# Kernel tuning notes

Measured on AMD Instinct MI355X. Metric: run time of the kernel, lower is better.

## Reference

```python
import jax, jax.numpy as jnp
import numpy as np

N_POINTS = 2097152
N_LEVELS = 16
F_PER_LEVEL = 2
LOG2_T = 19
T = 1 << LOG2_T            # 524288 entries per level
BASE_RES = 16
GROWTH = 1.5
PRIME_Y = np.uint32(2654435761)  # tcnn 2D spatial-hash prime (dim 0 prime is 1)


def _level_encode(x, tab, level):
    """Bilinear hash-grid lookup for one level. x: [N,2] in [0,1], tab: [T,F]."""
    scale = BASE_RES * GROWTH ** level - 1.0          # python float, static
    res = int(np.ceil(scale)) + 1                     # grid resolution (static)
    dense = res * res <= T                            # tcnn: dense if grid fits

    pos = x * jnp.asarray(scale, x.dtype) + 0.5       # [N,2]
    pg = jnp.floor(pos)
    frac = pos - pg                                   # [N,2] interpolation weights
    pg = pg.astype(jnp.uint32)

    out = jnp.zeros((x.shape[0], F_PER_LEVEL), x.dtype)
    for dx in (0, 1):
        for dy in (0, 1):
            cx = pg[:, 0] + np.uint32(dx)
            cy = pg[:, 1] + np.uint32(dy)
            if dense:
                idx = (cx + cy * np.uint32(res)) % np.uint32(T)
            else:
                idx = (cx ^ (cy * PRIME_Y)) % np.uint32(T)
            wx = frac[:, 0] if dx else 1.0 - frac[:, 0]
            wy = frac[:, 1] if dy else 1.0 - frac[:, 1]
            out = out + tab[idx.astype(jnp.int32)] * (wx * wy)[:, None]
    return out  # [N, F]


def setup_inputs() -> dict:
    key = jax.random.key(0)
    k1, k2 = jax.random.split(key)
    x = jax.random.uniform(k1, (N_POINTS, 2), dtype=jnp.float32)
    # tcnn initializes hash-grid params uniform in [-1e-4, 1e-4]
    table = jax.random.uniform(k2, (N_LEVELS, T, F_PER_LEVEL), dtype=jnp.float32,
                               minval=-1e-4, maxval=1e-4)
    return {"x": x, "table": table}


def reference(x, table):
    # multiresolution hash encoding: per-level bilinear gather, concat features
    outs = [_level_encode(x, table[l], l) for l in range(N_LEVELS)]
    return jnp.concatenate(outs, axis=-1)  # [N, N_LEVELS * F_PER_LEVEL] = [N, 32]
```

## Files before the change

### kernel.cpp

```cpp
#include <hip/hip_runtime.h>
#include <stdint.h>


constexpr int      kNPoints = 2097152;
constexpr uint32_t kT       = 524288u;
constexpr uint32_t kTMask   = kT - 1u;
constexpr uint32_t kPrimeY  = 2654435761u;

typedef float vf4 __attribute__((ext_vector_type(4)));

__device__ __forceinline__ float2 nt_load_f2(const float2* p) {
    union { unsigned long long u; float2 f2; } u;
    u.u = __builtin_nontemporal_load(reinterpret_cast<const unsigned long long*>(p));
    return u.f2;
}

__device__ __forceinline__ void nt_store_f2(float2* p, float2 v) {
    union { unsigned long long u; float2 f2; } u; u.f2 = v;
    __builtin_nontemporal_store(u.u, reinterpret_cast<unsigned long long*>(p));
}

__device__ __forceinline__ void nt_store_f4(float* p, float a, float b, float c, float d) {
    vf4 v; v.x = a; v.y = b; v.z = c; v.w = d;
    __builtin_nontemporal_store(v, reinterpret_cast<vf4*>(p));
}

__device__ __host__ inline void level_consts(int l, float& sc, uint32_t& re, int& dense) {
    const float ksc[16] = {
        15.0f, 23.0f, 35.0f, 53.0f, 80.0f, 120.5f, 181.25f, 272.375f,
        409.0625f, 614.09375f, 921.640625f, 1382.9609375f,
        2074.94140625f, 3112.912109375f, 4669.8681640625f, 7005.30224609375f};
    const uint32_t kre[16] = {16u, 24u, 36u, 54u, 81u, 122u, 183u, 274u,
                              411u, 616u, 923u, 1384u, 2076u, 3114u, 4671u, 7007u};
    sc = ksc[l]; re = kre[l]; dense = (l < 10) ? 1 : 0;
}

__device__ __forceinline__ float2 encode_one(float2 xy, float scale, uint32_t res,
                                             int dense, const float2* __restrict__ tab) {
    const float px  = __fadd_rn(__fmul_rn(xy.x, scale), 0.5f);
    const float py  = __fadd_rn(__fmul_rn(xy.y, scale), 0.5f);
    const float fpx = floorf(px);
    const float fpy = floorf(py);
    const float fx  = px - fpx;
    const float fy  = py - fpy;
    const uint32_t gx = (uint32_t)fpx;
    const uint32_t gy = (uint32_t)fpy;

    float ax = 0.0f, ay = 0.0f;
#pragma unroll
    for (int dx = 0; dx < 2; ++dx) {
        const uint32_t cx = gx + (uint32_t)dx;
        const float    wx = dx ? fx : (1.0f - fx);
#pragma unroll
        for (int dy = 0; dy < 2; ++dy) {
            const uint32_t cy = gy + (uint32_t)dy;
            const float    wy = dy ? fy : (1.0f - fy);
            const uint32_t idx_d = (cx + cy * res) & kTMask;
            const uint32_t idx_h = (cx ^ (cy * kPrimeY)) & kTMask;
            const uint32_t idx   = dense ? idx_d : idx_h;
            const float2   v     = tab[idx];
            const float    w     = wx * wy;
            ax = fmaf(v.x, w, ax);
            ay = fmaf(v.y, w, ay);
        }
    }
    return make_float2(ax, ay);
}

__global__ __launch_bounds__(256) void hash8_kernel(
    const float* __restrict__ x,
    const float* __restrict__ table,
    float2* __restrict__ ws)
{
    const uint32_t slot  = blockIdx.x & 7u;
    const uint32_t chunk = blockIdx.x >> 3;
    const int      l     = 8 + (int)slot;
    float sc; uint32_t re; int de;
    level_consts(l, sc, re, de);
    const float2* __restrict__ tab =
        reinterpret_cast<const float2*>(table) + ((size_t)l << 19);
    float2* __restrict__ wsl = ws + (size_t)slot * kNPoints;

    const uint32_t base = chunk * 1024u + threadIdx.x;
    const float2* __restrict__ xv = reinterpret_cast<const float2*>(x);

    float2 xy[4];
#pragma unroll
    for (int k = 0; k < 4; ++k)
        xy[k] = nt_load_f2(xv + base + (uint32_t)k * 256u);

    float2 r[4];
#pragma unroll
    for (int k = 0; k < 4; ++k)
        r[k] = encode_one(xy[k], sc, re, de, tab);

#pragma unroll
    for (int k = 0; k < 4; ++k)
        nt_store_f2(wsl + base + (uint32_t)k * 256u, r[k]);
}

__global__ __launch_bounds__(256) void merge8_kernel(
    const float* __restrict__ x,
    const float* __restrict__ table,
    const float2* __restrict__ ws,
    float* __restrict__ out)
{
    __shared__ float s[128 * 36];
    const uint32_t tid = threadIdx.x;
    const uint32_t n   = blockIdx.x * 256u + tid;
    const float2   xy  = nt_load_f2(reinterpret_cast<const float2*>(x) + n);

    float2 r[16];
#pragma unroll
    for (int l = 0; l < 8; ++l) {
        float sc; uint32_t re; int de;
        level_consts(l, sc, re, de);
        const float2* tab = reinterpret_cast<const float2*>(table) + ((size_t)l << 19);
        r[l] = encode_one(xy, sc, re, de, tab);
    }
#pragma unroll
    for (int j = 0; j < 8; ++j)
        r[8 + j] = nt_load_f2(ws + (size_t)j * kNPoints + n);

#pragma unroll
    for (int h = 0; h < 2; ++h) {
        if ((tid >> 7) == (uint32_t)h) {
            const uint32_t p = tid & 127u;
#pragma unroll
            for (int l = 0; l < 16; ++l) {
                s[p * 36 + 2 * l]     = r[l].x;
                s[p * 36 + 2 * l + 1] = r[l].y;
            }
        }
        __syncthreads();
        float* ob = out + (size_t)blockIdx.x * 8192 + (uint32_t)h * 4096u;
#pragma unroll
        for (int k = 0; k < 4; ++k) {
            const uint32_t q   = tid + (uint32_t)k * 256u;
            const uint32_t row = q >> 3;
            const uint32_t c   = (q & 7u) * 4u;
            const float* sp = &s[row * 36 + c];
            nt_store_f4(ob + q * 4u, sp[0], sp[1], sp[2], sp[3]);
        }
        if (h == 0) __syncthreads();
    }
}

__global__ __launch_bounds__(256) void hashgrid_fwd_fallback(
    const float* __restrict__ x,
    const float* __restrict__ table,
    float* __restrict__ out)
{
    const uint32_t tid = blockIdx.x * blockDim.x + threadIdx.x;
    const uint32_t l   = tid & 15u;
    const uint32_t n   = tid >> 4;
    float sc; uint32_t re; int de;
    level_consts((int)l, sc, re, de);
    const float2 xy = reinterpret_cast<const float2*>(x)[n];
    const float2* tab = reinterpret_cast<const float2*>(table) + ((size_t)l << 19);
    const float2 r = encode_one(xy, sc, re, de, tab);
    reinterpret_cast<float2*>(out)[tid] = r;
}

extern "C" void kernel_launch(void* const* d_in, const int* in_sizes, int n_in,
                              void* d_out, int out_size, void* d_ws, size_t ws_size,
                              hipStream_t stream) {
    const float* x     = (const float*)d_in[0];
    const float* table = (const float*)d_in[1];
    float*       out   = (float*)d_out;

    const size_t need8 = (size_t)8 * kNPoints * sizeof(float2);

    if (ws_size >= need8) {
        float2* ws = (float2*)d_ws;
        hash8_kernel<<<16384, 256, 0, stream>>>(x, table, ws);
        merge8_kernel<<<kNPoints / 256, 256, 0, stream>>>(x, table, ws, out);
    } else {
        hashgrid_fwd_fallback<<<(kNPoints * 16) / 256, 256, 0, stream>>>(x, table, out);
    }
}
```

Baseline: 686.8 us.

## Use paired 16-byte loads for dense levels and single-pass LDS transpose

For dense levels, the x and x+1 corners are now fetched together as one 16-byte load per row, cutting four gathers to two. Hashed levels compute the corner indices with a shared prime product and issue all gathers before any accumulation. The merge kernel now stages all 256 points in a larger LDS tile with a single barrier. It also drops the nontemporal hints on x, workspace and output accesses. The paired load assumes the two adjacent entries never wrap past the table mask, which holds for these dense resolutions. The larger LDS tile may lower occupancy.

Result: slower. 732.4 us (+6.6%).

```diff
diff --git a/kernel.cpp b/kernel.cpp
--- a/kernel.cpp
+++ b/kernel.cpp
@@ -7,8 +7,6 @@
 constexpr uint32_t kTMask   = kT - 1u;
 constexpr uint32_t kPrimeY  = 2654435761u;
 
-typedef float vf4 __attribute__((ext_vector_type(4)));
-
 __device__ __forceinline__ float2 nt_load_f2(const float2* p) {
     union { unsigned long long u; float2 f2; } u;
     u.u = __builtin_nontemporal_load(reinterpret_cast<const unsigned long long*>(p));
@@ -20,9 +18,11 @@
     __builtin_nontemporal_store(u.u, reinterpret_cast<unsigned long long*>(p));
 }
 
-__device__ __forceinline__ void nt_store_f4(float* p, float a, float b, float c, float d) {
-    vf4 v; v.x = a; v.y = b; v.z = c; v.w = d;
-    __builtin_nontemporal_store(v, reinterpret_cast<vf4*>(p));
+struct PairLd { float2 lo, hi; };
+__device__ __forceinline__ PairLd load_pair(const float2* __restrict__ p) {
+    PairLd r;
+    __builtin_memcpy(&r, p, 16);
+    return r;
 }
 
 __device__ __host__ inline void level_consts(int l, float& sc, uint32_t& re, int& dense) {
@@ -35,35 +35,43 @@
     sc = ksc[l]; re = kre[l]; dense = (l < 10) ? 1 : 0;
 }
 
-__device__ __forceinline__ float2 encode_one(float2 xy, float scale, uint32_t res,
-                                             int dense, const float2* __restrict__ tab) {
+__device__ __forceinline__ void setup_pt(float2 xy, float scale,
+                                         uint32_t& gx, uint32_t& gy,
+                                         float& fx, float& fy) {
     const float px  = __fadd_rn(__fmul_rn(xy.x, scale), 0.5f);
     const float py  = __fadd_rn(__fmul_rn(xy.y, scale), 0.5f);
     const float fpx = floorf(px);
     const float fpy = floorf(py);
-    const float fx  = px - fpx;
-    const float fy  = py - fpy;
-    const uint32_t gx = (uint32_t)fpx;
-    const uint32_t gy = (uint32_t)fpy;
-
-    float ax = 0.0f, ay = 0.0f;
-#pragma unroll
-    for (int dx = 0; dx < 2; ++dx) {
-        const uint32_t cx = gx + (uint32_t)dx;
-        const float    wx = dx ? fx : (1.0f - fx);
-#pragma unroll
-        for (int dy = 0; dy < 2; ++dy) {
-            const uint32_t cy = gy + (uint32_t)dy;
-            const float    wy = dy ? fy : (1.0f - fy);
-            const uint32_t idx_d = (cx + cy * res) & kTMask;
-            const uint32_t idx_h = (cx ^ (cy * kPrimeY)) & kTMask;
-            const uint32_t idx   = dense ? idx_d : idx_h;
-            const float2   v     = tab[idx];
-            const float    w     = wx * wy;
-            ax = fmaf(v.x, w, ax);
-            ay = fmaf(v.y, w, ay);
-        }
-    }
+    fx = px - fpx;
+    fy = py - fpy;
+    gx = (uint32_t)fpx;
+    gy = (uint32_t)fpy;
+}
+
+__device__ __forceinline__ float2 acc_pairs(PairLd A, PairLd B, float fx, float fy) {
+    const float w00 = (1.0f - fx) * (1.0f - fy);
+    const float w01 = (1.0f - fx) * fy;
+    const float w10 = fx * (1.0f - fy);
+    const float w11 = fx * fy;
+    float ax = fmaf(A.lo.x, w00, 0.0f);
+    float ay = fmaf(A.lo.y, w00, 0.0f);
+    ax = fmaf(B.lo.x, w01, ax); ay = fmaf(B.lo.y, w01, ay);
+    ax = fmaf(A.hi.x, w10, ax); ay = fmaf(A.hi.y, w10, ay);
+    ax = fmaf(B.hi.x, w11, ax); ay = fmaf(B.hi.y, w11, ay);
+    return make_float2(ax, ay);
+}
+
+__device__ __forceinline__ float2 acc_quad(float2 v00, float2 v01, float2 v10, float2 v11,
+                                           float fx, float fy) {
+    const float w00 = (1.0f - fx) * (1.0f - fy);
+    const float w01 = (1.0f - fx) * fy;
+    const float w10 = fx * (1.0f - fy);
+    const float w11 = fx * fy;
+    float ax = fmaf(v00.x, w00, 0.0f);
+    float ay = fmaf(v00.y, w00, 0.0f);
+    ax = fmaf(v01.x, w01, ax); ay = fmaf(v01.y, w01, ay);
+    ax = fmaf(v10.x, w10, ax); ay = fmaf(v10.y, w10, ay);
+    ax = fmaf(v11.x, w11, ax); ay = fmaf(v11.y, w11, ay);
     return make_float2(ax, ay);
 }
 
@@ -89,60 +97,92 @@
     for (int k = 0; k < 4; ++k)
         xy[k] = nt_load_f2(xv + base + (uint32_t)k * 256u);
 
+    uint32_t gx[4], gy[4];
+    float    fx[4], fy[4];
+#pragma unroll
+    for (int k = 0; k < 4; ++k)
+        setup_pt(xy[k], sc, gx[k], gy[k], fx[k], fy[k]);
+
     float2 r[4];
-#pragma unroll
-    for (int k = 0; k < 4; ++k)
-        r[k] = encode_one(xy[k], sc, re, de, tab);
+    if (de) {
+        PairLd A[4], B[4];
+#pragma unroll
+        for (int k = 0; k < 4; ++k) {
+            const uint32_t i00 = gx[k] + gy[k] * re;
+            A[k] = load_pair(tab + i00);
+            B[k] = load_pair(tab + i00 + re);
+        }
+#pragma unroll
+        for (int k = 0; k < 4; ++k)
+            r[k] = acc_pairs(A[k], B[k], fx[k], fy[k]);
+    } else {
+        float2 v[4][4];
+#pragma unroll
+        for (int k = 0; k < 4; ++k) {
+            const uint32_t cx = gx[k];
+            const uint32_t K0 = gy[k] * kPrimeY;
+            const uint32_t K1 = K0 + kPrimeY;
+            v[k][0] = tab[(cx ^ K0) & kTMask];
+            v[k][1] = tab[(cx ^ K1) & kTMask];
+            v[k][2] = tab[((cx + 1u) ^ K0) & kTMask];
+            v[k][3] = tab[((cx + 1u) ^ K1) & kTMask];
+        }
+#pragma unroll
+        for (int k = 0; k < 4; ++k)
+            r[k] = acc_quad(v[k][0], v[k][1], v[k][2], v[k][3], fx[k], fy[k]);
+    }
 
 #pragma unroll
     for (int k = 0; k < 4; ++k)
         nt_store_f2(wsl + base + (uint32_t)k * 256u, r[k]);
 }
 
-__global__ __launch_bounds__(256) void merge8_kernel(
+__global__ __launch_bounds__(256) void merge_kernel(
     const float* __restrict__ x,
     const float* __restrict__ table,
     const float2* __restrict__ ws,
     float* __restrict__ out)
 {
-    __shared__ float s[128 * 36];
+    __shared__ float s[256 * 36];
     const uint32_t tid = threadIdx.x;
     const uint32_t n   = blockIdx.x * 256u + tid;
-    const float2   xy  = nt_load_f2(reinterpret_cast<const float2*>(x) + n);
-
-    float2 r[16];
+    const float2   xy  = reinterpret_cast<const float2*>(x)[n];
+
+    float fx[8], fy[8];
+    PairLd A[8], B[8];
 #pragma unroll
     for (int l = 0; l < 8; ++l) {
         float sc; uint32_t re; int de;
         level_consts(l, sc, re, de);
         const float2* tab = reinterpret_cast<const float2*>(table) + ((size_t)l << 19);
-        r[l] = encode_one(xy, sc, re, de, tab);
-    }
+        uint32_t gx, gy;
+        setup_pt(xy, sc, gx, gy, fx[l], fy[l]);
+        const uint32_t i00 = gx + gy * re;
+        A[l] = load_pair(tab + i00);
+        B[l] = load_pair(tab + i00 + re);
+    }
+    float2 wv[8];
 #pragma unroll
     for (int j = 0; j < 8; ++j)
-        r[8 + j] = nt_load_f2(ws + (size_t)j * kNPoints + n);
-
-#pragma unroll
-    for (int h = 0; h < 2; ++h) {
-        if ((tid >> 7) == (uint32_t)h) {
-            const uint32_t p = tid & 127u;
-#pragma unroll
-            for (int l = 0; l < 16; ++l) {
-                s[p * 36 + 2 * l]     = r[l].x;
-                s[p * 36 + 2 * l + 1] = r[l].y;
-            }
-        }
-        __syncthreads();
-        float* ob = out + (size_t)blockIdx.x * 8192 + (uint32_t)h * 4096u;
-#pragma unroll
-        for (int k = 0; k < 4; ++k) {
-            const uint32_t q   = tid + (uint32_t)k * 256u;
-            const uint32_t row = q >> 3;
-            const uint32_t c   = (q & 7u) * 4u;
-            const float* sp = &s[row * 36 + c];
-            nt_store_f4(ob + q * 4u, sp[0], sp[1], sp[2], sp[3]);
-        }
-        if (h == 0) __syncthreads();
+        wv[j] = ws[(size_t)j * kNPoints + n];
+
+    float2* srow = reinterpret_cast<float2*>(&s[tid * 36]);
+#pragma unroll
+    for (int l = 0; l < 8; ++l)
+        srow[l] = acc_pairs(A[l], B[l], fx[l], fy[l]);
+#pragma unroll
+    for (int j = 0; j < 8; ++j)
+        srow[8 + j] = wv[j];
+    __syncthreads();
+
+    float4* outb = reinterpret_cast<float4*>(out + (size_t)blockIdx.x * 8192);
+#pragma unroll
+    for (int k = 0; k < 8; ++k) {
+        const uint32_t q   = tid + (uint32_t)k * 256u;
+        const uint32_t row = q >> 3;
+        const uint32_t c   = (q & 7u) * 4u;
+        const float* sp = &s[row * 36 + c];
+        outb[q] = make_float4(sp[0], sp[1], sp[2], sp[3]);
     }
 }
 
@@ -158,7 +198,21 @@
     level_consts((int)l, sc, re, de);
     const float2 xy = reinterpret_cast<const float2*>(x)[n];
     const float2* tab = reinterpret_cast<const float2*>(table) + ((size_t)l << 19);
-    const float2 r = encode_one(xy, sc, re, de, tab);
+    uint32_t gx, gy; float fx, fy;
+    setup_pt(xy, sc, gx, gy, fx, fy);
+    float2 v00, v01, v10, v11;
+    if (de) {
+        const uint32_t i00 = gx + gy * re;
+        v00 = tab[i00]; v10 = tab[i00 + 1u];
+        v01 = tab[i00 + re]; v11 = tab[i00 + re + 1u];
+    } else {
+        const uint32_t K0 = gy * kPrimeY, K1 = K0 + kPrimeY;
+        v00 = tab[(gx ^ K0) & kTMask];
+        v01 = tab[(gx ^ K1) & kTMask];
+        v10 = tab[((gx + 1u) ^ K0) & kTMask];
+        v11 = tab[((gx + 1u) ^ K1) & kTMask];
+    }
+    const float2 r = acc_quad(v00, v01, v10, v11, fx, fy);
     reinterpret_cast<float2*>(out)[tid] = r;
 }
 
@@ -174,7 +228,7 @@
     if (ws_size >= need8) {
         float2* ws = (float2*)d_ws;
         hash8_kernel<<<16384, 256, 0, stream>>>(x, table, ws);
-        merge8_kernel<<<kNPoints / 256, 256, 0, stream>>>(x, table, ws, out);
+        merge_kernel<<<kNPoints / 256, 256, 0, stream>>>(x, table, ws, out);
     } else {
         hashgrid_fwd_fallback<<<(kNPoints * 16) / 256, 256, 0, stream>>>(x, table, out);
     }
```

## Use 16-byte table loads in hash8 and single-pass LDS transpose in merge

Applied to the files above, without the earlier changes.

The hash8 kernel now gathers table entries as float4 (16-byte) loads and picks the needed half. It also splits the dense and hashed paths into separate loops and computes the dense index without the modulo mask. The merge kernel stages all 256 points in a larger shared buffer with one sync instead of two half-passes. It also replaces the nontemporal loads and stores with ordinary ones. Wider loads double the bytes fetched per gather in exchange for possibly better cache-line behaviour. The larger LDS footprint may reduce occupancy.

Measured after the change: 738.3 us. 1.08x slower.

```diff
diff --git a/kernel.cpp b/kernel.cpp
--- a/kernel.cpp
+++ b/kernel.cpp
@@ -7,8 +7,6 @@
 constexpr uint32_t kTMask   = kT - 1u;
 constexpr uint32_t kPrimeY  = 2654435761u;
 
-typedef float vf4 __attribute__((ext_vector_type(4)));
-
 __device__ __forceinline__ float2 nt_load_f2(const float2* p) {
     union { unsigned long long u; float2 f2; } u;
     u.u = __builtin_nontemporal_load(reinterpret_cast<const unsigned long long*>(p));
@@ -18,11 +16,6 @@
 __device__ __forceinline__ void nt_store_f2(float2* p, float2 v) {
     union { unsigned long long u; float2 f2; } u; u.f2 = v;
     __builtin_nontemporal_store(u.u, reinterpret_cast<unsigned long long*>(p));
-}
-
-__device__ __forceinline__ void nt_store_f4(float* p, float a, float b, float c, float d) {
-    vf4 v; v.x = a; v.y = b; v.z = c; v.w = d;
-    __builtin_nontemporal_store(v, reinterpret_cast<vf4*>(p));
 }
 
 __device__ __host__ inline void level_consts(int l, float& sc, uint32_t& re, int& dense) {
@@ -33,6 +26,38 @@
     const uint32_t kre[16] = {16u, 24u, 36u, 54u, 81u, 122u, 183u, 274u,
                               411u, 616u, 923u, 1384u, 2076u, 3114u, 4671u, 7007u};
     sc = ksc[l]; re = kre[l]; dense = (l < 10) ? 1 : 0;
+}
+
+__device__ __forceinline__ void setup_pt(float2 xy, float scale,
+                                         uint32_t& gx, uint32_t& gy,
+                                         float& fx, float& fy) {
+    const float px  = __fadd_rn(__fmul_rn(xy.x, scale), 0.5f);
+    const float py  = __fadd_rn(__fmul_rn(xy.y, scale), 0.5f);
+    const float fpx = floorf(px);
+    const float fpy = floorf(py);
+    fx = px - fpx;
+    fy = py - fpy;
+    gx = (uint32_t)fpx;
+    gy = (uint32_t)fpy;
+}
+
+__device__ __forceinline__ float2 acc_quad(float2 v00, float2 v01, float2 v10, float2 v11,
+                                           float fx, float fy) {
+    const float w00 = (1.0f - fx) * (1.0f - fy);
+    const float w01 = (1.0f - fx) * fy;
+    const float w10 = fx * (1.0f - fy);
+    const float w11 = fx * fy;
+    float ax = fmaf(v00.x, w00, 0.0f);
+    float ay = fmaf(v00.y, w00, 0.0f);
+    ax = fmaf(v01.x, w01, ax); ay = fmaf(v01.y, w01, ay);
+    ax = fmaf(v10.x, w10, ax); ay = fmaf(v10.y, w10, ay);
+    ax = fmaf(v11.x, w11, ax); ay = fmaf(v11.y, w11, ay);
+    return make_float2(ax, ay);
+}
+
+__device__ __forceinline__ float2 entry16(const float4* __restrict__ tab4, uint32_t idx) {
+    const float4 P = tab4[idx >> 1];
+    return (idx & 1u) ? make_float2(P.z, P.w) : make_float2(P.x, P.y);
 }
 
 __device__ __forceinline__ float2 encode_one(float2 xy, float scale, uint32_t res,
@@ -77,8 +102,8 @@
     const int      l     = 8 + (int)slot;
     float sc; uint32_t re; int de;
     level_consts(l, sc, re, de);
-    const float2* __restrict__ tab =
-        reinterpret_cast<const float2*>(table) + ((size_t)l << 19);
+    const float4* __restrict__ tab4 = reinterpret_cast<const float4*>(
+        reinterpret_cast<const float2*>(table) + ((size_t)l << 19));
     float2* __restrict__ wsl = ws + (size_t)slot * kNPoints;
 
     const uint32_t base = chunk * 1024u + threadIdx.x;
@@ -90,59 +115,74 @@
         xy[k] = nt_load_f2(xv + base + (uint32_t)k * 256u);
 
     float2 r[4];
-#pragma unroll
-    for (int k = 0; k < 4; ++k)
-        r[k] = encode_one(xy[k], sc, re, de, tab);
+    if (de) {
+#pragma unroll
+        for (int k = 0; k < 4; ++k) {
+            uint32_t gx, gy; float fx, fy;
+            setup_pt(xy[k], sc, gx, gy, fx, fy);
+            const uint32_t i00 = gx + gy * re;
+            const float2 v00 = entry16(tab4, i00);
+            const float2 v10 = entry16(tab4, i00 + 1u);
+            const float2 v01 = entry16(tab4, i00 + re);
+            const float2 v11 = entry16(tab4, i00 + re + 1u);
+            r[k] = acc_quad(v00, v01, v10, v11, fx, fy);
+        }
+    } else {
+#pragma unroll
+        for (int k = 0; k < 4; ++k) {
+            uint32_t gx, gy; float fx, fy;
+            setup_pt(xy[k], sc, gx, gy, fx, fy);
+            const uint32_t K0 = gy * kPrimeY;
+            const uint32_t K1 = K0 + kPrimeY;
+            const float2 v00 = entry16(tab4, (gx        ^ K0) & kTMask);
+            const float2 v10 = entry16(tab4, ((gx + 1u) ^ K0) & kTMask);
+            const float2 v01 = entry16(tab4, (gx        ^ K1) & kTMask);
+            const float2 v11 = entry16(tab4, ((gx + 1u) ^ K1) & kTMask);
+            r[k] = acc_quad(v00, v01, v10, v11, fx, fy);
+        }
+    }
 
 #pragma unroll
     for (int k = 0; k < 4; ++k)
         nt_store_f2(wsl + base + (uint32_t)k * 256u, r[k]);
 }
 
-__global__ __launch_bounds__(256) void merge8_kernel(
+__global__ __launch_bounds__(256) void merge_kernel(
     const float* __restrict__ x,
     const float* __restrict__ table,
     const float2* __restrict__ ws,
     float* __restrict__ out)
 {
-    __shared__ float s[128 * 36];
+    __shared__ float s[256 * 36];
     const uint32_t tid = threadIdx.x;
     const uint32_t n   = blockIdx.x * 256u + tid;
-    const float2   xy  = nt_load_f2(reinterpret_cast<const float2*>(x) + n);
-
-    float2 r[16];
+    const float2   xy  = reinterpret_cast<const float2*>(x)[n];
+
 #pragma unroll
     for (int l = 0; l < 8; ++l) {
         float sc; uint32_t re; int de;
         level_consts(l, sc, re, de);
         const float2* tab = reinterpret_cast<const float2*>(table) + ((size_t)l << 19);
-        r[l] = encode_one(xy, sc, re, de, tab);
-    }
-#pragma unroll
-    for (int j = 0; j < 8; ++j)
-        r[8 + j] = nt_load_f2(ws + (size_t)j * kNPoints + n);
-
-#pragma unroll
-    for (int h = 0; h < 2; ++h) {
-        if ((tid >> 7) == (uint32_t)h) {
-            const uint32_t p = tid & 127u;
-#pragma unroll
-            for (int l = 0; l < 16; ++l) {
-                s[p * 36 + 2 * l]     = r[l].x;
-                s[p * 36 + 2 * l + 1] = r[l].y;
-            }
-        }
-        __syncthreads();
-        float* ob = out + (size_t)blockIdx.x * 8192 + (uint32_t)h * 4096u;
-#pragma unroll
-        for (int k = 0; k < 4; ++k) {
-            const uint32_t q   = tid + (uint32_t)k * 256u;
-            const uint32_t row = q >> 3;
-            const uint32_t c   = (q & 7u) * 4u;
-            const float* sp = &s[row * 36 + c];
-            nt_store_f4(ob + q * 4u, sp[0], sp[1], sp[2], sp[3]);
-        }
-        if (h == 0) __syncthreads();
+        const float2 r = encode_one(xy, sc, re, de, tab);
+        s[tid * 36 + 2 * l]     = r.x;
+        s[tid * 36 + 2 * l + 1] = r.y;
+    }
+#pragma unroll
+    for (int j = 0; j < 8; ++j) {
+        const float2 v = ws[(size_t)j * kNPoints + n];
+        s[tid * 36 + 2 * (8 + j)]     = v.x;
+        s[tid * 36 + 2 * (8 + j) + 1] = v.y;
+    }
+    __syncthreads();
+
+    float4* outb = reinterpret_cast<float4*>(out + (size_t)blockIdx.x * 8192);
+#pragma unroll
+    for (int k = 0; k < 8; ++k) {
+        const uint32_t q   = tid + (uint32_t)k * 256u;
+        const uint32_t row = q >> 3;
+        const uint32_t c   = (q & 7u) * 4u;
+        const float* sp = &s[row * 36 + c];
+        outb[q] = make_float4(sp[0], sp[1], sp[2], sp[3]);
     }
 }
 
@@ -174,7 +214,7 @@
     if (ws_size >= need8) {
         float2* ws = (float2*)d_ws;
         hash8_kernel<<<16384, 256, 0, stream>>>(x, table, ws);
-        merge8_kernel<<<kNPoints / 256, 256, 0, stream>>>(x, table, ws, out);
+        merge_kernel<<<kNPoints / 256, 256, 0, stream>>>(x, table, ws, out);
     } else {
         hashgrid_fwd_fallback<<<(kNPoints * 16) / 256, 256, 0, stream>>>(x, table, out);
     }
```
